# Kernel optimization log

Measured on AMD Instinct MI355X. Metric: run time of the kernel, lower is better.

Reference implementation:

```python
import jax, jax.numpy as jnp
import numpy as np

DIM = 1024
EPS = 1e-5

def layer_norm(x, gamma, beta):
    mu = jnp.mean(x, axis=-1, keepdims=True)
    var = jnp.mean(jnp.square(x - mu), axis=-1, keepdims=True)
    return (x - mu) * jax.lax.rsqrt(var + EPS) * gamma + beta

def setup_inputs() -> dict:
    key = jax.random.key(0)
    k1, k2 = jax.random.split(key)
    B, Nv, Nt = 8, 4096, 4096
    visual_tokens = jax.random.normal(k1, (B, Nv, DIM), dtype=jnp.float32)
    text_tokens = jax.random.normal(k2, (B, Nt, DIM), dtype=jnp.float32)
    gamma_v = jnp.ones((DIM,), dtype=jnp.float32)
    beta_v = jnp.zeros((DIM,), dtype=jnp.float32)
    gamma_t = jnp.ones((DIM,), dtype=jnp.float32)
    beta_t = jnp.zeros((DIM,), dtype=jnp.float32)
    return {"visual_tokens": visual_tokens, "text_tokens": text_tokens,
            "gamma_v": gamma_v, "beta_v": beta_v,
            "gamma_t": gamma_t, "beta_t": beta_t}

def reference(visual_tokens, text_tokens, gamma_v, beta_v, gamma_t, beta_t):
    # Dual LayerNorm
    V = layer_norm(visual_tokens, gamma_v, beta_v)   # [B, Nv, D]
    T = layer_norm(text_tokens, gamma_t, beta_t)     # [B, Nt, D]
    scale = jnp.sqrt(jnp.asarray(DIM, dtype=V.dtype))  # note: sqrt(dim), per source
    scores = jnp.einsum('bvd,btd->bvt', V, T) / scale  # [B, Nv, Nt]
    attn = jax.nn.softmax(scores, axis=-1)
    out = jnp.einsum('bvt,btd->bvd', attn, T)          # [B, Nv, D]
    return out
```

## Files before the change

kernel.cpp:

```cpp
#include <hip/hip_runtime.h>
#include <hip/hip_bf16.h>
#include <stdint.h>

#define DIMD 1024
#define NSEQ 4096
#define BATCH 8
#define LN_EPS 1e-5f

typedef __attribute__((ext_vector_type(8))) short bf16x8;
typedef __attribute__((ext_vector_type(4))) float f32x4;

__device__ __forceinline__ ushort f2bf(float f) {
  union { __hip_bfloat16 h; ushort u; } cv;
  cv.h = __float2bfloat16(f);
  return cv.u;
}

__device__ __forceinline__ void gload16(const void* g, void* l) {
  __builtin_amdgcn_global_load_lds(
      (const __attribute__((address_space(1))) uint32_t*)g,
      (__attribute__((address_space(3))) uint32_t*)l, 16, 0, 0);
}

#define MIDBAR()   asm volatile("s_barrier" ::: "memory")
#define ENDBAR()   asm volatile("s_waitcnt lgkmcnt(0)\n\ts_barrier" ::: "memory")
#define ENDBARV4() asm volatile("s_waitcnt vmcnt(4) lgkmcnt(0)\n\ts_barrier" ::: "memory")
#define ENDBARV0() asm volatile("s_waitcnt vmcnt(0) lgkmcnt(0)\n\ts_barrier" ::: "memory")

__device__ __forceinline__ int swz64(int byte) {
  return byte ^ (((byte >> 7) & 3) << 4);
}

__global__ __launch_bounds__(256) void ln_bf16_kernel(
    const float* __restrict__ x, const float* __restrict__ gamma,
    const float* __restrict__ beta, ushort* __restrict__ y, float scale)
{
  const int lane = threadIdx.x & 63;
  const int wv   = threadIdx.x >> 6;
  const size_t row = (size_t)blockIdx.x * 4 + wv;
  const float* xr = x + row * DIMD;

  float4 v[4];
#pragma unroll
  for (int c = 0; c < 4; ++c)
    v[c] = *(const float4*)(xr + c * 256 + lane * 4);

  float s = 0.f;
#pragma unroll
  for (int c = 0; c < 4; ++c) s += v[c].x + v[c].y + v[c].z + v[c].w;
#pragma unroll
  for (int m = 32; m >= 1; m >>= 1) s += __shfl_xor(s, m, 64);
  const float mean = s * (1.0f / DIMD);

  float vs = 0.f;
#pragma unroll
  for (int c = 0; c < 4; ++c) {
    float a0 = v[c].x - mean, a1 = v[c].y - mean;
    float a2 = v[c].z - mean, a3 = v[c].w - mean;
    vs += a0 * a0 + a1 * a1 + a2 * a2 + a3 * a3;
  }
#pragma unroll
  for (int m = 32; m >= 1; m >>= 1) vs += __shfl_xor(vs, m, 64);
  const float rstd = rsqrtf(vs * (1.0f / DIMD) + LN_EPS);

  ushort* yr = y + row * DIMD;
#pragma unroll
  for (int c = 0; c < 4; ++c) {
    const int d = c * 256 + lane * 4;
    float4 g  = *(const float4*)(gamma + d);
    float4 bb = *(const float4*)(beta + d);
    ushort4 o;
    o.x = f2bf(((v[c].x - mean) * rstd * g.x + bb.x) * scale);
    o.y = f2bf(((v[c].y - mean) * rstd * g.y + bb.y) * scale);
    o.z = f2bf(((v[c].z - mean) * rstd * g.z + bb.z) * scale);
    o.w = f2bf(((v[c].w - mean) * rstd * g.w + bb.w) * scale);
    *(ushort4*)(yr + d) = o;
  }
}

__global__ __launch_bounds__(256) void transpose_kernel(
    const ushort* __restrict__ src, ushort* __restrict__ dst)
{
  __shared__ ushort tile[64][72];
  const int t   = threadIdx.x;
  const int bid = blockIdx.x;
  const int b   = bid >> 10;
  const int rem = bid & 1023;
  const int n0  = (rem >> 4) << 6;
  const int d0  = (rem & 15) << 6;
  const ushort* sb = src + ((size_t)b * NSEQ) * DIMD;
  ushort* db       = dst + ((size_t)b * DIMD) * NSEQ;

#pragma unroll
  for (int k = 0; k < 2; ++k) {
    int c = t + 256 * k;
    int r = c >> 3, scol = (c & 7) * 8;
    *(uint4*)&tile[r][scol] =
        *(const uint4*)(sb + (size_t)(n0 + r) * DIMD + d0 + scol);
  }
  __syncthreads();
#pragma unroll
  for (int k = 0; k < 2; ++k) {
    int c = t + 256 * k;
    int dr = c >> 3, ns = (c & 7) * 8;
    union { ushort u[8]; uint4 q; } tv;
#pragma unroll
    for (int i = 0; i < 8; ++i) tv.u[i] = tile[ns + i][dr];
    *(uint4*)(db + (size_t)(d0 + dr) * NSEQ + n0 + ns) = tv.q;
  }
}


__device__ __forceinline__ void stage_chunk(const ushort* __restrict__ g,
                                            int ld, char* l, int tid) {
  const int o0 = tid * 16;
  const int o1 = o0 + 8192;
  const int s0 = swz64(o0);
  const int s1 = swz64(o1);
  gload16(g + (size_t)(s0 >> 6) * ld + ((s0 & 63) >> 1), l + o0);
  gload16(g + (size_t)(s1 >> 6) * ld + ((s1 & 63) >> 1), l + o1);
}

__device__ __forceinline__ bf16x8 ldsw_read(const char* base, int row, int lg) {
  return *(const bf16x8*)(base + swz64(row * 64 + lg * 16));
}

__device__ __forceinline__ void read_af(const char* Ac, int wm, int mh,
                                        int l15, int lg, bf16x8 (&af)[4]) {
#pragma unroll
  for (int m = 0; m < 4; ++m)
    af[m] = ldsw_read(Ac, wm * 128 + (mh * 4 + m) * 16 + l15, lg);
}
__device__ __forceinline__ void read_bf(const char* Bc, int wn,
                                        int l15, int lg, bf16x8 (&bf)[4]) {
#pragma unroll
  for (int n = 0; n < 4; ++n)
    bf[n] = ldsw_read(Bc, wn * 64 + n * 16 + l15, lg);
}

__device__ __forceinline__ void gemm_core_256(
    const ushort* __restrict__ Ab, const ushort* __restrict__ Bb,
    int lda, int ldb, int NT, char* smem, f32x4 (&acc)[8][4],
    int tid, int wm, int wn, int l15, int lg)
{
  stage_chunk(Ab,      lda, smem + 0,     tid);
  stage_chunk(Bb,      ldb, smem + 32768, tid);
  stage_chunk(Ab + 32, lda, smem + 16384, tid);
  stage_chunk(Bb + 32, ldb, smem + 49152, tid);
  ENDBARV4();

  for (int kt = 0; kt < NT; ++kt) {
    char* cb = smem + (kt & 1) * 65536;
    char* nbuf = smem + (((kt & 1) ^ 1) * 65536);
    const ushort* An = Ab + (size_t)(kt + 1) * 64;
    const ushort* Bn = Bb + (size_t)(kt + 1) * 64;
    const bool pf = (kt + 1 < NT);
    const char* A0 = cb;
    const char* A1 = cb + 16384;
    const char* B0 = cb + 32768;
    const char* B1 = cb + 49152;
    bf16x8 af[4], bf[4];

    read_af(A0, wm, 0, l15, lg, af);
    read_bf(B0, wn, l15, lg, bf);
    if (pf) stage_chunk(An, lda, nbuf + 0, tid);
    MIDBAR();
    __builtin_amdgcn_s_setprio(1);
#pragma unroll
    for (int m = 0; m < 4; ++m)
#pragma unroll
      for (int n = 0; n < 4; ++n)
        acc[m][n] = __builtin_amdgcn_mfma_f32_16x16x32_bf16(af[m], bf[n], acc[m][n], 0, 0, 0);
    __builtin_amdgcn_s_setprio(0);
    ENDBAR();

    read_af(A0, wm, 1, l15, lg, af);
    if (pf) stage_chunk(Bn, ldb, nbuf + 32768, tid);
    MIDBAR();
    __builtin_amdgcn_s_setprio(1);
#pragma unroll
    for (int m = 0; m < 4; ++m)
#pragma unroll
      for (int n = 0; n < 4; ++n)
        acc[4 + m][n] = __builtin_amdgcn_mfma_f32_16x16x32_bf16(af[m], bf[n], acc[4 + m][n], 0, 0, 0);
    __builtin_amdgcn_s_setprio(0);
    if (pf) { ENDBARV4(); } else { ENDBARV0(); }

    read_af(A1, wm, 0, l15, lg, af);
    read_bf(B1, wn, l15, lg, bf);
    if (pf) stage_chunk(An + 32, lda, nbuf + 16384, tid);
    MIDBAR();
    __builtin_amdgcn_s_setprio(1);
#pragma unroll
    for (int m = 0; m < 4; ++m)
#pragma unroll
      for (int n = 0; n < 4; ++n)
        acc[m][n] = __builtin_amdgcn_mfma_f32_16x16x32_bf16(af[m], bf[n], acc[m][n], 0, 0, 0);
    __builtin_amdgcn_s_setprio(0);
    ENDBAR();

    read_af(A1, wm, 1, l15, lg, af);
    if (pf) stage_chunk(Bn + 32, ldb, nbuf + 49152, tid);
    MIDBAR();
    __builtin_amdgcn_s_setprio(1);
#pragma unroll
    for (int m = 0; m < 4; ++m)
#pragma unroll
      for (int n = 0; n < 4; ++n)
        acc[4 + m][n] = __builtin_amdgcn_mfma_f32_16x16x32_bf16(af[m], bf[n], acc[4 + m][n], 0, 0, 0);
    __builtin_amdgcn_s_setprio(0);
    if (pf) { ENDBARV4(); } else { ENDBAR(); }
  }
}

__global__ __launch_bounds__(512, 2) void gemm1_256(
    const ushort* __restrict__ Q, const ushort* __restrict__ K,
    ushort* __restrict__ S, float* __restrict__ Rsum,
    int b0, size_t s_stride)
{
  extern __shared__ char smem[];
  const int tid  = threadIdx.x;
  const int lane = tid & 63;
  const int wave = tid >> 6;
  const int wm = wave >> 2, wn = wave & 3;
  const int l15 = lane & 15, lg = lane >> 4;

  int bx, by, bzc;
  if (gridDim.z == BATCH) {
    const int hw = blockIdx.x + (blockIdx.y << 4) + (blockIdx.z << 8);
    bzc = hw & 7;
    const int inner = hw >> 3;
    bx = inner & 15; by = (inner >> 4) & 15;
  } else {
    bx = blockIdx.x; by = blockIdx.y; bzc = 0;
  }

  const int bz   = b0 + bzc;
  const int row0 = by * 256, col0 = bx * 256;
  const ushort* Qb = Q + (size_t)bz * NSEQ * DIMD + (size_t)row0 * DIMD;
  const ushort* Kb = K + (size_t)bz * NSEQ * DIMD + (size_t)col0 * DIMD;

  f32x4 acc[8][4];
#pragma unroll
  for (int m = 0; m < 8; ++m)
#pragma unroll
    for (int n = 0; n < 4; ++n) acc[m][n] = 0.0f;

  gemm_core_256(Kb, Qb, DIMD, DIMD, DIMD / 64, smem, acc, tid, wm, wn, l15, lg);

  ushort* Sb = S + (size_t)bzc * s_stride;
  float*  Rs = Rsum + (size_t)bz * NSEQ;
  float vsum[4] = {0.f, 0.f, 0.f, 0.f};
#pragma unroll
  for (int ti = 0; ti < 8; ++ti) {
#pragma unroll
    for (int vi = 0; vi < 4; ++vi) {
      const int v = row0 + wn * 64 + vi * 16 + l15;
      const int t = col0 + wm * 128 + ti * 16 + lg * 4;
      float p0 = __expf(acc[ti][vi][0]);
      float p1 = __expf(acc[ti][vi][1]);
      float p2 = __expf(acc[ti][vi][2]);
      float p3 = __expf(acc[ti][vi][3]);
      vsum[vi] += (p0 + p1) + (p2 + p3);
      unsigned long long pk =
          (unsigned long long)f2bf(p0)        |
          ((unsigned long long)f2bf(p1) << 16) |
          ((unsigned long long)f2bf(p2) << 32) |
          ((unsigned long long)f2bf(p3) << 48);
      *(unsigned long long*)(Sb + (size_t)v * NSEQ + t) = pk;
    }
  }
#pragma unroll
  for (int vi = 0; vi < 4; ++vi) {
    float s = vsum[vi];
    s += __shfl_xor(s, 16, 64);
    s += __shfl_xor(s, 32, 64);
    if (lg == 0)
      atomicAdd(Rs + row0 + wn * 64 + vi * 16 + l15, s);
  }
}

__global__ __launch_bounds__(512, 2) void gemm2_256(
    const ushort* __restrict__ S, const ushort* __restrict__ Kt,
    const float* __restrict__ Rsum, float* __restrict__ Out,
    int b0, size_t s_stride)
{
  extern __shared__ char smem[];
  const int tid  = threadIdx.x;
  const int lane = tid & 63;
  const int wave = tid >> 6;
  const int wm = wave >> 2, wn = wave & 3;
  const int l15 = lane & 15, lg = lane >> 4;

  int bx, by, bzc;
  if (gridDim.z == BATCH) {
    const int hw = blockIdx.x + (blockIdx.y << 2) + (blockIdx.z << 6);
    bzc = hw & 7;
    const int inner = hw >> 3;
    bx = inner & 3; by = inner >> 2;
  } else {
    bx = blockIdx.x; by = blockIdx.y; bzc = 0;
  }

  const int bz   = b0 + bzc;
  const int row0 = by * 256;
  const int col0 = bx * 256;
  const ushort* Sb2 = S  + (size_t)bzc * s_stride + (size_t)row0 * NSEQ;
  const ushort* Vtb = Kt + ((size_t)bz * DIMD + col0) * NSEQ;

  f32x4 acc[8][4];
#pragma unroll
  for (int m = 0; m < 8; ++m)
#pragma unroll
    for (int n = 0; n < 4; ++n) acc[m][n] = 0.0f;

  gemm_core_256(Vtb, Sb2, NSEQ, NSEQ, NSEQ / 64, smem, acc, tid, wm, wn, l15, lg);

  const float* Rs = Rsum + (size_t)bz * NSEQ;
  float* Ob = Out + (size_t)bz * NSEQ * DIMD;
  float inv[4];
#pragma unroll
  for (int vi = 0; vi < 4; ++vi)
    inv[vi] = 1.0f / Rs[row0 + wn * 64 + vi * 16 + l15];
#pragma unroll
  for (int di = 0; di < 8; ++di) {
#pragma unroll
    for (int vi = 0; vi < 4; ++vi) {
      const int v = row0 + wn * 64 + vi * 16 + l15;
      const int d = col0 + wm * 128 + di * 16 + lg * 4;
      f32x4 o = acc[di][vi] * inv[vi];
      __builtin_nontemporal_store(
          o, (f32x4*)(Ob + (size_t)v * DIMD + d));
    }
  }
}

extern "C" void kernel_launch(void* const* d_in, const int* in_sizes, int n_in,
                              void* d_out, int out_size, void* d_ws, size_t ws_size,
                              hipStream_t stream) {
  const float* vis = (const float*)d_in[0];
  const float* txt = (const float*)d_in[1];
  const float* gv  = (const float*)d_in[2];
  const float* bv  = (const float*)d_in[3];
  const float* gt  = (const float*)d_in[4];
  const float* bt  = (const float*)d_in[5];
  float* out = (float*)d_out;

  const size_t tokens = (size_t)BATCH * NSEQ * DIMD;
  ushort* Qbf = (ushort*)d_ws;
  ushort* Kbf = Qbf + tokens;
  ushort* Ktb = Kbf + tokens;
  char*   wsb = (char*)d_ws;
  float*  Rsum = (float*)(wsb + 201326592);
  ushort* Sbuf = (ushort*)(wsb + 201457664);

  const size_t S_FULL = (size_t)BATCH * NSEQ * NSEQ * 2;
  const size_t NEED_FULL = 201457664 + S_FULL;

  ln_bf16_kernel<<<BATCH * NSEQ / 4, 256, 0, stream>>>(vis, gv, bv, Qbf, 0.03125f);
  ln_bf16_kernel<<<BATCH * NSEQ / 4, 256, 0, stream>>>(txt, gt, bt, Kbf, 1.0f);
  transpose_kernel<<<BATCH * (NSEQ / 64) * (DIMD / 64), 256, 0, stream>>>(Kbf, Ktb);

  hipFuncSetAttribute((const void*)gemm1_256,
                      hipFuncAttributeMaxDynamicSharedMemorySize, 131072);
  hipFuncSetAttribute((const void*)gemm2_256,
                      hipFuncAttributeMaxDynamicSharedMemorySize, 131072);

  hipMemsetAsync(Rsum, 0, (size_t)BATCH * NSEQ * sizeof(float), stream);

  if (ws_size >= NEED_FULL) {
    gemm1_256<<<dim3(16, 16, BATCH), 512, 131072, stream>>>(
        Qbf, Kbf, Sbuf, Rsum, 0, (size_t)NSEQ * NSEQ);
    gemm2_256<<<dim3(4, 16, BATCH), 512, 131072, stream>>>(
        Sbuf, Ktb, Rsum, out, 0, (size_t)NSEQ * NSEQ);
  } else {
    for (int b = 0; b < BATCH; ++b) {
      gemm1_256<<<dim3(16, 16, 1), 512, 131072, stream>>>(
          Qbf, Kbf, Sbuf, Rsum, b, 0);
      gemm2_256<<<dim3(4, 16, 1), 512, 131072, stream>>>(
          Sbuf, Ktb, Rsum, out, b, 0);
    }
  }
}
```

Baseline: 670.5 us.

## Deepen GEMM LDS pipeline with staggered half-tile prefetch and unroll by two

Restructures the bf16 GEMM main loop to unroll two K-tiles per iteration, using fixed buffer addresses. The prologue stages one and a half tiles instead of one, and each LDS quarter is refilled as soon as it has been consumed. The aim is to keep more global-to-LDS loads in flight, hiding memory latency behind the MFMA work and reducing waits at barriers. It assumes NT is even, and the vmcnt counts must line up with the new staging order or data races can occur.

```diff
diff --git a/kernel.cpp b/kernel.cpp
--- a/kernel.cpp
+++ b/kernel.cpp
@@ -138,78 +138,88 @@
     bf[n] = ldsw_read(Bc, wn * 64 + n * 16 + l15, lg);
 }
 
+#define MFMA16(BASE)                                                          \
+  do {                                                                        \
+    MIDBAR();                                                                 \
+    __builtin_amdgcn_s_setprio(1);                                            \
+    _Pragma("unroll")                                                         \
+    for (int m = 0; m < 4; ++m)                                               \
+      _Pragma("unroll")                                                       \
+      for (int n = 0; n < 4; ++n)                                             \
+        acc[(BASE) + m][n] = __builtin_amdgcn_mfma_f32_16x16x32_bf16(         \
+            af[m], bf[n], acc[(BASE) + m][n], 0, 0, 0);                       \
+    __builtin_amdgcn_s_setprio(0);                                            \
+  } while (0)
+
 __device__ __forceinline__ void gemm_core_256(
     const ushort* __restrict__ Ab, const ushort* __restrict__ Bb,
     int lda, int ldb, int NT, char* smem, f32x4 (&acc)[8][4],
     int tid, int wm, int wn, int l15, int lg)
 {
-  stage_chunk(Ab,      lda, smem + 0,     tid);
-  stage_chunk(Bb,      ldb, smem + 32768, tid);
-  stage_chunk(Ab + 32, lda, smem + 16384, tid);
-  stage_chunk(Bb + 32, ldb, smem + 49152, tid);
-  ENDBARV4();
-
-  for (int kt = 0; kt < NT; ++kt) {
-    char* cb = smem + (kt & 1) * 65536;
-    char* nbuf = smem + (((kt & 1) ^ 1) * 65536);
-    const ushort* An = Ab + (size_t)(kt + 1) * 64;
-    const ushort* Bn = Bb + (size_t)(kt + 1) * 64;
-    const bool pf = (kt + 1 < NT);
-    const char* A0 = cb;
-    const char* A1 = cb + 16384;
-    const char* B0 = cb + 32768;
-    const char* B1 = cb + 49152;
+  char* buf0 = smem;
+  char* buf1 = smem + 65536;
+
+  stage_chunk(Ab,      lda, buf0 + 0,     tid);
+  stage_chunk(Bb,      ldb, buf0 + 32768, tid);
+  stage_chunk(Ab + 32, lda, buf0 + 16384, tid);
+  stage_chunk(Bb + 32, ldb, buf0 + 49152, tid);
+  stage_chunk(Ab + 64, lda, buf1 + 0,     tid);
+  stage_chunk(Bb + 64, ldb, buf1 + 32768, tid);
+  asm volatile("s_waitcnt vmcnt(4)\n\ts_barrier" ::: "memory");
+
+  for (int T = 0; T < NT; T += 2) {
+    const bool pf = (T + 2 < NT);
+    const ushort* A1s = Ab + (size_t)(T + 1) * 64;
+    const ushort* B1s = Bb + (size_t)(T + 1) * 64;
+    const ushort* A2s = Ab + (size_t)(T + 2) * 64;
+    const ushort* B2s = Bb + (size_t)(T + 2) * 64;
+    const ushort* A3s = Ab + (size_t)(T + 3) * 64;
+    const ushort* B3s = Bb + (size_t)(T + 3) * 64;
     bf16x8 af[4], bf[4];
 
-    read_af(A0, wm, 0, l15, lg, af);
-    read_bf(B0, wn, l15, lg, bf);
-    if (pf) stage_chunk(An, lda, nbuf + 0, tid);
-    MIDBAR();
-    __builtin_amdgcn_s_setprio(1);
-#pragma unroll
-    for (int m = 0; m < 4; ++m)
-#pragma unroll
-      for (int n = 0; n < 4; ++n)
-        acc[m][n] = __builtin_amdgcn_mfma_f32_16x16x32_bf16(af[m], bf[n], acc[m][n], 0, 0, 0);
-    __builtin_amdgcn_s_setprio(0);
-    ENDBAR();
-
-    read_af(A0, wm, 1, l15, lg, af);
-    if (pf) stage_chunk(Bn, ldb, nbuf + 32768, tid);
-    MIDBAR();
-    __builtin_amdgcn_s_setprio(1);
-#pragma unroll
-    for (int m = 0; m < 4; ++m)
-#pragma unroll
-      for (int n = 0; n < 4; ++n)
-        acc[4 + m][n] = __builtin_amdgcn_mfma_f32_16x16x32_bf16(af[m], bf[n], acc[4 + m][n], 0, 0, 0);
-    __builtin_amdgcn_s_setprio(0);
+    read_af(buf0 + 0, wm, 0, l15, lg, af);
+    read_bf(buf0 + 32768, wn, l15, lg, bf);
+    stage_chunk(A1s + 32, lda, buf1 + 16384, tid);
+    MFMA16(0);
+    ENDBAR();
+
+    read_af(buf0 + 0, wm, 1, l15, lg, af);
+    stage_chunk(B1s + 32, ldb, buf1 + 49152, tid);
+    MFMA16(4);
+    ENDBAR();
+
+    read_af(buf0 + 16384, wm, 0, l15, lg, af);
+    read_bf(buf0 + 49152, wn, l15, lg, bf);
+    if (pf) stage_chunk(A2s, lda, buf0 + 0, tid);
+    MFMA16(0);
+    ENDBAR();
+
+    read_af(buf0 + 16384, wm, 1, l15, lg, af);
+    if (pf) stage_chunk(B2s, ldb, buf0 + 32768, tid);
+    MFMA16(4);
     if (pf) { ENDBARV4(); } else { ENDBARV0(); }
 
-    read_af(A1, wm, 0, l15, lg, af);
-    read_bf(B1, wn, l15, lg, bf);
-    if (pf) stage_chunk(An + 32, lda, nbuf + 16384, tid);
-    MIDBAR();
-    __builtin_amdgcn_s_setprio(1);
-#pragma unroll
-    for (int m = 0; m < 4; ++m)
-#pragma unroll
-      for (int n = 0; n < 4; ++n)
-        acc[m][n] = __builtin_amdgcn_mfma_f32_16x16x32_bf16(af[m], bf[n], acc[m][n], 0, 0, 0);
-    __builtin_amdgcn_s_setprio(0);
-    ENDBAR();
-
-    read_af(A1, wm, 1, l15, lg, af);
-    if (pf) stage_chunk(Bn + 32, ldb, nbuf + 49152, tid);
-    MIDBAR();
-    __builtin_amdgcn_s_setprio(1);
-#pragma unroll
-    for (int m = 0; m < 4; ++m)
-#pragma unroll
-      for (int n = 0; n < 4; ++n)
-        acc[4 + m][n] = __builtin_amdgcn_mfma_f32_16x16x32_bf16(af[m], bf[n], acc[4 + m][n], 0, 0, 0);
-    __builtin_amdgcn_s_setprio(0);
-    if (pf) { ENDBARV4(); } else { ENDBAR(); }
+    read_af(buf1 + 0, wm, 0, l15, lg, af);
+    read_bf(buf1 + 32768, wn, l15, lg, bf);
+    if (pf) stage_chunk(A2s + 32, lda, buf0 + 16384, tid);
+    MFMA16(0);
+    ENDBAR();
+
+    read_af(buf1 + 0, wm, 1, l15, lg, af);
+    if (pf) stage_chunk(B2s + 32, ldb, buf0 + 49152, tid);
+    MFMA16(4);
+    ENDBAR();
+
+    read_af(buf1 + 16384, wm, 0, l15, lg, af);
+    read_bf(buf1 + 49152, wn, l15, lg, bf);
+    if (pf) stage_chunk(A3s, lda, buf1 + 0, tid);
+    MFMA16(0);
+    ENDBAR();
+
+    read_af(buf1 + 16384, wm, 1, l15, lg, af);
+    if (pf) stage_chunk(B3s, ldb, buf1 + 32768, tid);
+    MFMA16(4);
+    if (pf) { ENDBARV4(); } else { ENDBARV0(); }
   }
 }
 
```

After: 815.1 us. 1.22x slower.
